# Kernel tuning notes

Measured on AMD Instinct MI355X. Metric: run time of the kernel, lower is better.

The kernel has to match this reference:

```python
import jax, jax.numpy as jnp
import numpy as np

THRESH = 0.5   # matching_threshold
EPS = 1e-8     # torch.cosine_similarity eps
LN_EPS = 1e-5

B, N = 32, 256
ID, PD, VD, SD = 2048, 768, 1024, 8


def _linear_block(x, w1, b1, w2, b2):
    # LinearBlock with linear_layer_num=2, dropout=0 (eval)
    h = jax.nn.relu(x @ w1 + b1)
    return h @ w2 + b2


def _layernorm(x, g, b):
    m = jnp.mean(x, axis=-1, keepdims=True)
    v = jnp.var(x, axis=-1, keepdims=True)
    return (x - m) / jnp.sqrt(v + LN_EPS) * g + b


def _greedy_match(sim_b, mask_b, prev_feat_b, prev_sp_b):
    # sim_b: [N, N] cosine similarities, mask_b: [N, N] bool
    n = sim_b.shape[0]
    iota = jnp.arange(n)

    def step(visited, inp):
        sim_i, mask_i = inp
        valid = mask_i & (~visited) & (sim_i >= THRESH)
        scores = jnp.where(valid, sim_i, -jnp.inf)
        idx = jnp.argmax(scores)          # first max, matching the torch loop
        found = jnp.any(valid)
        visited = visited | (found & (iota == idx))
        feat = jnp.where(found, prev_feat_b[idx], 0.0)
        sp = jnp.where(found, prev_sp_b[idx], 0.0)
        return visited, (feat, sp)

    _, (ofeat, osp) = jax.lax.scan(step, jnp.zeros((n,), bool), (sim_b, mask_b))
    return ofeat, osp


def setup_inputs() -> dict:
    key = jax.random.key(0)
    ks = jax.random.split(key, 32)
    s = 0.02
    inp = {
        'image_feature': jax.random.normal(ks[0], (B, N, ID), jnp.float32),
        'point_cloud_feature': jax.random.normal(ks[1], (B, N, PD), jnp.float32),
        'prev_image_feature': jax.random.normal(ks[2], (B, N, ID), jnp.float32),
        'prev_point_cloud_feature': jax.random.normal(ks[3], (B, N, PD), jnp.float32),
        'prev_spatial': jax.random.normal(ks[4], (B, N, SD), jnp.float32),
        'rel_dist_mask': jax.random.randint(ks[5], (B, N, N), 0, 2).astype(bool),
        # img_fusion: LinearBlock(2*ID, ID) -> Linear(ID, VD) -> LayerNorm(VD)
        'iw1': jax.random.normal(ks[6], (2 * ID, ID), jnp.float32) * s,
        'ib1': jnp.zeros((ID,), jnp.float32),
        'iw2': jax.random.normal(ks[7], (ID, ID), jnp.float32) * s,
        'ib2': jnp.zeros((ID,), jnp.float32),
        'iw3': jax.random.normal(ks[8], (ID, VD), jnp.float32) * s,
        'ib3': jnp.zeros((VD,), jnp.float32),
        'ig': jnp.ones((VD,), jnp.float32),
        'ibeta': jnp.zeros((VD,), jnp.float32),
        # pc_fusion: LinearBlock(2*PD, PD) -> Linear(PD, VD) -> LayerNorm(VD)
        'pw1': jax.random.normal(ks[9], (2 * PD, PD), jnp.float32) * s,
        'pb1': jnp.zeros((PD,), jnp.float32),
        'pw2': jax.random.normal(ks[10], (PD, PD), jnp.float32) * s,
        'pb2': jnp.zeros((PD,), jnp.float32),
        'pw3': jax.random.normal(ks[11], (PD, VD), jnp.float32) * s,
        'pb3': jnp.zeros((VD,), jnp.float32),
        'pg': jnp.ones((VD,), jnp.float32),
        'pbeta': jnp.zeros((VD,), jnp.float32),
        # linear: LinearBlock(2*VD, VD) -> LayerNorm(VD)
        'fw1': jax.random.normal(ks[12], (2 * VD, VD), jnp.float32) * s,
        'fb1': jnp.zeros((VD,), jnp.float32),
        'fw2': jax.random.normal(ks[13], (VD, VD), jnp.float32) * s,
        'fb2': jnp.zeros((VD,), jnp.float32),
        'fg': jnp.ones((VD,), jnp.float32),
        'fbeta': jnp.zeros((VD,), jnp.float32),
    }
    return inp


def reference(image_feature, point_cloud_feature, prev_image_feature,
              prev_point_cloud_feature, prev_spatial, rel_dist_mask,
              iw1, ib1, iw2, ib2, iw3, ib3, ig, ibeta,
              pw1, pb1, pw2, pb2, pw3, pb3, pg, pbeta,
              fw1, fb1, fw2, fb2, fg, fbeta):
    # ---- matching_previous_objects (batched cosine sim + greedy scan) ----
    feat = jnp.concatenate([image_feature, point_cloud_feature], axis=2)       # [B,N,D]
    prev_feat = jnp.concatenate([prev_image_feature, prev_point_cloud_feature], axis=2)
    fn = feat / jnp.maximum(jnp.linalg.norm(feat, axis=-1, keepdims=True), EPS)
    pn = prev_feat / jnp.maximum(jnp.linalg.norm(prev_feat, axis=-1, keepdims=True), EPS)
    sim = jnp.einsum('bid,bjd->bij', fn, pn)                                    # [B,N,N]
    ordered_prev, new_prev_spatial = jax.vmap(_greedy_match)(
        sim, rel_dist_mask, prev_feat, prev_spatial)
    prev_img = ordered_prev[:, :, :ID]
    prev_pc = ordered_prev[:, :, ID:]
    # ---- fusion MLPs ----
    img = jnp.concatenate([image_feature, prev_img], axis=2)
    img = _layernorm(_linear_block(img, iw1, ib1, iw2, ib2) @ iw3 + ib3, ig, ibeta)
    pc = jnp.concatenate([point_cloud_feature, prev_pc], axis=2)
    pc = _layernorm(_linear_block(pc, pw1, pb1, pw2, pb2) @ pw3 + pb3, pg, pbeta)
    vis = jnp.concatenate([img, pc], axis=2)
    vis = _layernorm(_linear_block(vis, fw1, fb1, fw2, fb2), fg, fbeta)
    return vis, new_prev_spatial
```

## Files before the change

### kernel.cpp

```cpp
#include <hip/hip_runtime.h>
#include <math.h>

#define Bn 32
#define Nn 256
#define IDIM 2048
#define PDIM 768
#define VDIM 1024
#define SDIM 8
#define D2 2816
#define Mrows 8192
#define EPSN 1e-8f
#define LNEPS 1e-5f
#define THRESH 0.5f

typedef unsigned short u16;
typedef __attribute__((ext_vector_type(8))) short bf16x8;
typedef __attribute__((ext_vector_type(4))) float f32x4;

__device__ __forceinline__ u16 f2b(float f) {
    unsigned u = __float_as_uint(f);
    unsigned r = (u + 0x7FFFu + ((u >> 16) & 1u)) >> 16;
    return (u16)r;
}

__device__ __forceinline__ void gload16(const void* g, void* l) {
    __builtin_amdgcn_global_load_lds(
        (const __attribute__((address_space(1))) unsigned*)g,
        (__attribute__((address_space(3))) unsigned*)l, 16, 0, 0);
}

#define VMWAIT4 asm volatile("s_waitcnt vmcnt(4)" ::: "memory")
#define VMWAIT2 asm volatile("s_waitcnt vmcnt(2)" ::: "memory")
#define VMWAIT0 asm volatile("s_waitcnt vmcnt(0)" ::: "memory")
#define BAR() do { __builtin_amdgcn_s_barrier(); __builtin_amdgcn_sched_barrier(0); } while (0)
#define PRIO1 __builtin_amdgcn_s_setprio(1)
#define PRIO0 __builtin_amdgcn_s_setprio(0)

__global__ __launch_bounds__(256) void pack_k(
    const float* __restrict__ img, const float* __restrict__ pc,
    const float* __restrict__ pimg, const float* __restrict__ ppc,
    u16* __restrict__ featb, u16* __restrict__ pfeatb,
    float* __restrict__ nf, float* __restrict__ np_)
{
    const int row = blockIdx.x, t = threadIdx.x;
    const float* I = blockIdx.y ? pimg : img;
    const float* P = blockIdx.y ? ppc : pc;
    u16* O = blockIdx.y ? pfeatb : featb;
    float s = 0.f;
    const float4* I4 = (const float4*)(I + (size_t)row * IDIM);
    float4 a = I4[t * 2], b = I4[t * 2 + 1];
    s += a.x * a.x + a.y * a.y + a.z * a.z + a.w * a.w;
    s += b.x * b.x + b.y * b.y + b.z * b.z + b.w * b.w;
    u16* op = O + (size_t)row * D2 + t * 8;
    *(ushort4*)op       = make_ushort4(f2b(a.x), f2b(a.y), f2b(a.z), f2b(a.w));
    *(ushort4*)(op + 4) = make_ushort4(f2b(b.x), f2b(b.y), f2b(b.z), f2b(b.w));
    if (t < 192) {
        float4 c = ((const float4*)(P + (size_t)row * PDIM))[t];
        s += c.x * c.x + c.y * c.y + c.z * c.z + c.w * c.w;
        *(ushort4*)(O + (size_t)row * D2 + IDIM + t * 4) =
            make_ushort4(f2b(c.x), f2b(c.y), f2b(c.z), f2b(c.w));
    }
    for (int o = 32; o; o >>= 1) s += __shfl_down(s, o, 64);
    __shared__ float l4[4];
    if ((t & 63) == 0) l4[t >> 6] = s;
    __syncthreads();
    if (t == 0) (blockIdx.y ? np_ : nf)[row] = sqrtf(l4[0] + l4[1] + l4[2] + l4[3]);
}

__global__ __launch_bounds__(256) void twt_k(
    const float* __restrict__ W, u16* __restrict__ Wt, int K, int No)
{
    __shared__ float tb[32][33];
    const int tx = threadIdx.x & 31;
    const int ty = threadIdx.x >> 5;
    const int n0 = blockIdx.x * 32, k0 = blockIdx.y * 32;
#pragma unroll
    for (int qq = 0; qq < 4; ++qq)
        tb[ty + 8 * qq][tx] = W[(size_t)(k0 + ty + 8 * qq) * No + n0 + tx];
    __syncthreads();
#pragma unroll
    for (int qq = 0; qq < 4; ++qq)
        Wt[(size_t)(n0 + ty + 8 * qq) * K + k0 + tx] = f2b(tb[tx][ty + 8 * qq]);
}

template <int MODE, int RELU, int OUT>
__global__ __launch_bounds__(256) void mm_k(
    const u16* __restrict__ A, const u16* __restrict__ Aprev,
    const int* __restrict__ midx, const float* __restrict__ zbuf,
    int lda, int coff, int K1,
    const u16* __restrict__ Bt, int K,
    const float* __restrict__ bias,
    const float* __restrict__ nf, const float* __restrict__ np_,
    void* __restrict__ Cout, int ldc)
{
    __shared__ __align__(16) u16 Asm[4096];
    __shared__ __align__(16) u16 Bsm[4096];
    const int tid = threadIdx.x;
    const int wave = tid >> 6, lane = tid & 63;
    const int row0 = blockIdx.y * 128;
    const int cC0 = blockIdx.x * 128;
    const int brow0 = (OUT == 2 ? (row0 >> 8) * Nn : 0) + cC0;

    const int la = lane >> 2, q = lane & 3;
    const u16* pA0[2]; const u16* pB0[2];
    char* dstA[2]; char* dstB[2];
#pragma unroll
    for (int i = 0; i < 2; ++i) {
        int c = wave * 2 + i;
        int r = c * 16 + la;
        int sp = q ^ ((r >> 1) & 3);
        int grow = row0 + r;
        pA0[i] = A + (size_t)grow * lda + sp * 8;
        pB0[i] = Bt + (size_t)(brow0 + r) * K + sp * 8;
        dstA[i] = (char*)Asm + c * 1024;
        dstB[i] = (char*)Bsm + c * 1024;
    }

    const int wr = wave >> 1, wc = wave & 1;
    int aoff[4], boff[4];
#pragma unroll
    for (int m = 0; m < 4; ++m) {
        int r = wr * 64 + m * 16 + (lane & 15);
        aoff[m] = r * 64 + (((lane >> 4) ^ ((r >> 1) & 3)) << 4);
    }
#pragma unroll
    for (int n = 0; n < 4; ++n) {
        int c = wc * 64 + n * 16 + (lane & 15);
        boff[n] = c * 64 + (((lane >> 4) ^ ((c >> 1) & 3)) << 4);
    }

    f32x4 acc[4][4] = {};

    for (int k0 = 0; k0 < K; k0 += 32) {
#pragma unroll
        for (int i = 0; i < 2; ++i) {
            gload16(pA0[i] + k0, dstA[i]);
            gload16(pB0[i] + k0, dstB[i]);
        }
        __syncthreads();
        bf16x8 av[4], bv[4];
#pragma unroll
        for (int m = 0; m < 4; ++m) av[m] = *(const bf16x8*)((const char*)Asm + aoff[m]);
#pragma unroll
        for (int n = 0; n < 4; ++n) bv[n] = *(const bf16x8*)((const char*)Bsm + boff[n]);
#pragma unroll
        for (int m = 0; m < 4; ++m)
#pragma unroll
            for (int n = 0; n < 4; ++n)
                acc[m][n] = __builtin_amdgcn_mfma_f32_16x16x32_bf16(av[m], bv[n], acc[m][n], 0, 0, 0);
        __syncthreads();
    }

    const int rb = row0 + wr * 64;
    const int cl = cC0 + wc * 64 + (lane & 15);
    float sj[4];
#pragma unroll
    for (int n = 0; n < 4; ++n) {
        int bcol = brow0 + wc * 64 + n * 16 + (lane & 15);
        sj[n] = 1.f / fmaxf(np_[bcol], EPSN);
    }
#pragma unroll
    for (int m = 0; m < 4; ++m) {
#pragma unroll
        for (int n = 0; n < 4; ++n) {
            f32x4 v = acc[m][n];
#pragma unroll
            for (int rg = 0; rg < 4; ++rg) {
                int rr = rb + m * 16 + ((lane >> 4) << 2) + rg;
                float si = 1.f / fmaxf(nf[rr], EPSN);
                ((float*)Cout)[(size_t)rr * ldc + cl + n * 16] = v[rg] * si * sj[n];
            }
        }
    }
}

template <int MODE, int RELU, int OUT>
__global__ __launch_bounds__(512, 2) void mm8_k(
    const u16* __restrict__ A, const u16* __restrict__ Aprev,
    const int* __restrict__ midx, const u16* __restrict__ zb,
    int lda, int coff, int K1,
    const u16* __restrict__ Bt, int K,
    const float* __restrict__ bias,
    void* __restrict__ Cout, int ldc, int nblk)
{
    __shared__ __align__(16) u16 smem[65536];
    char* ldsv = (char*)smem;

    const int tid = threadIdx.x;
    const int wave = tid >> 6, lane = tid & 63;
    const int l15 = lane & 15, l4 = lane >> 4;
    const int wr = wave >> 2, wc = wave & 3;

    const int nwg = nblk * 32;
    const int orig = blockIdx.x;
    const int xcd = orig & 7, lid = orig >> 3;
    const int qq = nwg >> 3, rr8 = nwg & 7;
    const int swz = (xcd < rr8 ? xcd * (qq + 1) : rr8 * (qq + 1) + (xcd - rr8) * qq) + lid;
    const int row0 = (swz & 31) * 256;
    const int col0 = (swz >> 5) * 256;

    const u16* pA[2][2]; const u16* pA2[2][2]; const u16* pB[2][2];
    int cA8[2][2]; bool okA[2][2];
#pragma unroll
    for (int h = 0; h < 2; ++h)
#pragma unroll
        for (int i = 0; i < 2; ++i) {
            int lrow = (i * 512 + tid) >> 3;
            int r = h * 128 + lrow;
            int c = (tid & 7) ^ (lrow & 7);
            cA8[h][i] = c * 8;
            int grow = row0 + r;
            if (MODE == 0) {
                pA[h][i] = A + (size_t)grow * lda + c * 8;
                pA2[h][i] = nullptr; okA[h][i] = true;
            } else {
                pA[h][i] = A + (size_t)grow * lda + coff + c * 8;
                int jj = midx[grow];
                okA[h][i] = (jj >= 0);
                pA2[h][i] = okA[h][i]
                    ? (Aprev + (size_t)((grow & ~(Nn - 1)) + jj) * lda + coff + c * 8 - K1)
                    : (zb + c * 8);
            }
            pB[h][i] = Bt + (size_t)(col0 + r) * K + c * 8;
        }

#define STAGEA(h, kt, pp) do {                                                   \
    _Pragma("unroll")                                                            \
    for (int i_ = 0; i_ < 2; ++i_) {                                             \
        const u16* s_;                                                           \
        if (MODE == 0) s_ = pA[h][i_] + (kt);                                    \
        else {                                                                   \
            int gc_ = (kt) + cA8[h][i_];                                         \
            s_ = (gc_ < K1) ? (pA[h][i_] + (kt))                                 \
                            : (okA[h][i_] ? pA2[h][i_] + (kt) : pA2[h][i_]);     \
        }                                                                        \
        gload16(s_, ldsv + ((pp) * 32768 + (h) * 16384 + i_ * 8192 + wave * 1024)); \
    }                                                                            \
} while (0)

#define STAGEB(h, kt, pp) do {                                                   \
    _Pragma("unroll")                                                            \
    for (int i_ = 0; i_ < 2; ++i_)                                               \
        gload16(pB[h][i_] + (kt),                                                \
                ldsv + (65536 + (pp) * 32768 + (h) * 16384 + i_ * 8192 + wave * 1024)); \
} while (0)

    int aoffs[8][2], boffs[4][2];
#pragma unroll
    for (int m = 0; m < 8; ++m) {
        int r = m * 32 + wr * 16 + l15;
#pragma unroll
        for (int ks = 0; ks < 2; ++ks)
            aoffs[m][ks] = r * 128 + (((ks * 4 + l4) ^ (lane & 7)) << 4);
    }
#pragma unroll
    for (int n = 0; n < 4; ++n) {
        int r = n * 64 + wc * 16 + l15;
#pragma unroll
        for (int ks = 0; ks < 2; ++ks)
            boffs[n][ks] = r * 128 + (((ks * 4 + l4) ^ (lane & 7)) << 4);
    }

    bf16x8 avc[4][2], bvc[2][2];
    f32x4 acc[8][4] = {};

#define READA(mh, base) do {                                                     \
    _Pragma("unroll")                                                            \
    for (int m_ = 0; m_ < 4; ++m_) {                                             \
        avc[m_][0] = *(const bf16x8*)((base) + aoffs[(mh) * 4 + m_][0]);         \
        avc[m_][1] = *(const bf16x8*)((base) + aoffs[(mh) * 4 + m_][1]);         \
    }                                                                            \
} while (0)

#define READB(nh, base) do {                                                     \
    _Pragma("unroll")                                                            \
    for (int n_ = 0; n_ < 2; ++n_) {                                             \
        bvc[n_][0] = *(const bf16x8*)((base) + boffs[(nh) * 2 + n_][0]);         \
        bvc[n_][1] = *(const bf16x8*)((base) + boffs[(nh) * 2 + n_][1]);         \
    }                                                                            \
} while (0)

#define MFMA16(mh, nh) do {                                                      \
    _Pragma("unroll")                                                            \
    for (int ks_ = 0; ks_ < 2; ++ks_)                                            \
    _Pragma("unroll")                                                            \
    for (int m_ = 0; m_ < 4; ++m_)                                               \
    _Pragma("unroll")                                                            \
    for (int n_ = 0; n_ < 2; ++n_)                                               \
        acc[(mh) * 4 + m_][(nh) * 2 + n_] = __builtin_amdgcn_mfma_f32_16x16x32_bf16( \
            avc[m_][ks_], bvc[n_][ks_], acc[(mh) * 4 + m_][(nh) * 2 + n_], 0, 0, 0); \
} while (0)

    const int nt = K >> 6;

    STAGEA(0, 0, 0); STAGEB(0, 0, 0); STAGEA(1, 0, 0); STAGEB(1, 0, 0);

    int t = 0;
    for (; t < nt - 1; ++t) {
        const int p = t & 1;
        const char* bA = ldsv + p * 32768;
        const char* bB = ldsv + 65536 + p * 32768;
        const int kn = (t + 1) << 6;
        VMWAIT4; BAR();
        STAGEA(0, kn, p ^ 1);
        READA(0, bA); READB(0, bB);
        PRIO1; MFMA16(0, 0); PRIO0;
        VMWAIT4; BAR();
        STAGEB(0, kn, p ^ 1);
        READA(1, bA);
        PRIO1; MFMA16(1, 0); PRIO0;
        VMWAIT4; BAR();
        STAGEA(1, kn, p ^ 1);
        READB(1, bB);
        PRIO1; MFMA16(1, 1); PRIO0;
        BAR();
        STAGEB(1, kn, p ^ 1);
        READA(0, bA);
        PRIO1; MFMA16(0, 1); PRIO0;
    }
    {
        const int p = t & 1;
        const char* bA = ldsv + p * 32768;
        const char* bB = ldsv + 65536 + p * 32768;
        VMWAIT4; BAR(); READA(0, bA); READB(0, bB); PRIO1; MFMA16(0, 0); PRIO0;
        VMWAIT2; BAR(); READA(1, bA);               PRIO1; MFMA16(1, 0); PRIO0;
        VMWAIT0; BAR(); READB(1, bB);               PRIO1; MFMA16(1, 1); PRIO0;
        BAR();          READA(0, bA);               PRIO1; MFMA16(0, 1); PRIO0;
    }

#pragma unroll
    for (int n = 0; n < 4; ++n) {
        const int col = col0 + n * 64 + wc * 16 + l15;
        const float bz = bias[col];
#pragma unroll
        for (int m = 0; m < 8; ++m) {
#pragma unroll
            for (int rg = 0; rg < 4; ++rg) {
                int row = row0 + m * 32 + wr * 16 + l4 * 4 + rg;
                float x = acc[m][n][rg] + bz;
                if (RELU) x = fmaxf(x, 0.f);
                if (OUT == 0) ((u16*)Cout)[(size_t)row * ldc + col] = f2b(x);
                else          ((float*)Cout)[(size_t)row * ldc + col] = x;
            }
        }
    }
#undef STAGEA
#undef STAGEB
#undef READA
#undef READB
#undef MFMA16
}

__global__ __launch_bounds__(256) void match_k(
    const float* __restrict__ sim, const int* __restrict__ mask,
    const float* __restrict__ psp, int* __restrict__ midx,
    float* __restrict__ osp, float* __restrict__ zb)
{
    const int b = blockIdx.x;
    const int j = threadIdx.x;
    const int lane = j & 63, wid = j >> 6;
    __shared__ int vis[256];
    __shared__ unsigned long long wb[4];
    __shared__ float wv[4];
    __shared__ int wi[4];
    __shared__ int fidx_s;
    if (b == 0) zb[j] = 0.f;
    vis[j] = 0;
    __syncthreads();
    size_t rowoff = ((size_t)b * Nn) * Nn + j;
    float s = sim[rowoff];
    int mk = mask[rowoff];
    for (int i = 0; i < Nn; ++i) {
        float scur = s; int mkcur = mk;
        bool valid = mkcur && (!vis[j]) && (scur >= THRESH);
        if (i + 1 < Nn) {
            s = sim[rowoff + (size_t)(i + 1) * Nn];
            mk = mask[rowoff + (size_t)(i + 1) * Nn];
        }
        unsigned long long bal = __ballot(valid);
        if (lane == 0) wb[wid] = bal;
        __syncthreads();
        bool found = (wb[0] | wb[1] | wb[2] | wb[3]) != 0ULL;
        if (found) {
            float v = valid ? scur : -INFINITY;
            int idx = j;
            for (int o = 32; o; o >>= 1) {
                float v2 = __shfl_down(v, o, 64);
                int i2 = __shfl_down(idx, o, 64);
                if (v2 > v || (v2 == v && i2 < idx)) { v = v2; idx = i2; }
            }
            if (lane == 0) { wv[wid] = v; wi[wid] = idx; }
            __syncthreads();
            if (j == 0) {
                float bv = wv[0]; int bi = wi[0];
                for (int w = 1; w < 4; ++w)
                    if (wv[w] > bv || (wv[w] == bv && wi[w] < bi)) { bv = wv[w]; bi = wi[w]; }
                fidx_s = bi;
                vis[bi] = 1;
                midx[b * Nn + i] = bi;
            }
            __syncthreads();
            int fi = fidx_s;
            if (j < SDIM)
                osp[((size_t)b * Nn + i) * SDIM + j] = psp[((size_t)b * Nn + fi) * SDIM + j];
        } else {
            if (j == 0) midx[b * Nn + i] = -1;
            if (j < SDIM) osp[((size_t)b * Nn + i) * SDIM + j] = 0.f;
        }
        __syncthreads();
    }
}

template <int OB>
__global__ __launch_bounds__(256) void ln_k(
    const float* __restrict__ X, const float* __restrict__ g,
    const float* __restrict__ be, void* __restrict__ out,
    int ostride, int ooff)
{
    const int row = blockIdx.x, t = threadIdx.x;
    float4 v = *(const float4*)(X + (size_t)row * VDIM + t * 4);
    float s = v.x + v.y + v.z + v.w;
    __shared__ float l4[4];
    for (int o = 32; o; o >>= 1) s += __shfl_down(s, o, 64);
    if ((t & 63) == 0) l4[t >> 6] = s;
    __syncthreads();
    float mean = (l4[0] + l4[1] + l4[2] + l4[3]) * (1.f / VDIM);
    __syncthreads();
    float dx = v.x - mean, dy = v.y - mean, dz = v.z - mean, dw = v.w - mean;
    float qv = dx * dx + dy * dy + dz * dz + dw * dw;
    for (int o = 32; o; o >>= 1) qv += __shfl_down(qv, o, 64);
    if ((t & 63) == 0) l4[t >> 6] = qv;
    __syncthreads();
    float var = (l4[0] + l4[1] + l4[2] + l4[3]) * (1.f / VDIM);
    float rstd = rsqrtf(var + LNEPS);
    float4 gv = *(const float4*)(g + t * 4);
    float4 bv = *(const float4*)(be + t * 4);
    float ox = dx * rstd * gv.x + bv.x;
    float oy = dy * rstd * gv.y + bv.y;
    float oz = dz * rstd * gv.z + bv.z;
    float ow = dw * rstd * gv.w + bv.w;
    if (OB) {
        *(ushort4*)((u16*)out + (size_t)row * ostride + ooff + t * 4) =
            make_ushort4(f2b(ox), f2b(oy), f2b(oz), f2b(ow));
    } else {
        *(float4*)((float*)out + (size_t)row * ostride + ooff + t * 4) =
            make_float4(ox, oy, oz, ow);
    }
}

extern "C" void kernel_launch(void* const* d_in, const int* in_sizes, int n_in,
                              void* d_out, int out_size, void* d_ws, size_t ws_size,
                              hipStream_t stream)
{
    const float* image  = (const float*)d_in[0];
    const float* pcf    = (const float*)d_in[1];
    const float* pimage = (const float*)d_in[2];
    const float* ppcf   = (const float*)d_in[3];
    const float* psp    = (const float*)d_in[4];
    const int*   mask   = (const int*)d_in[5];
    const float* iw1 = (const float*)d_in[6];  const float* ib1 = (const float*)d_in[7];
    const float* iw2 = (const float*)d_in[8];  const float* ib2 = (const float*)d_in[9];
    const float* iw3 = (const float*)d_in[10]; const float* ib3 = (const float*)d_in[11];
    const float* ig  = (const float*)d_in[12]; const float* ibeta = (const float*)d_in[13];
    const float* pw1 = (const float*)d_in[14]; const float* pb1 = (const float*)d_in[15];
    const float* pw2 = (const float*)d_in[16]; const float* pb2 = (const float*)d_in[17];
    const float* pw3 = (const float*)d_in[18]; const float* pb3 = (const float*)d_in[19];
    const float* pg  = (const float*)d_in[20]; const float* pbeta = (const float*)d_in[21];
    const float* fw1 = (const float*)d_in[22]; const float* fb1 = (const float*)d_in[23];
    const float* fw2 = (const float*)d_in[24]; const float* fb2 = (const float*)d_in[25];
    const float* fg  = (const float*)d_in[26]; const float* fbeta = (const float*)d_in[27];

    float* out_vis = (float*)d_out;
    float* out_sp  = (float*)d_out + (size_t)Mrows * VDIM;

    char* w = (char*)d_ws;
    float* nf   = (float*)w; w += 32768;
    float* np_  = (float*)w; w += 32768;
    int*   midx = (int*)w;   w += 32768;
    u16*   Wt   = (u16*)w;   w += 16777216;
    u16*   featb  = (u16*)w; w += 46137344;
    u16*   pfeatb = (u16*)w; w += 46137344;
    char*  Creg = w; w += 33554432;
    char*  Dreg = w; w += 33554432;
    char*  Ereg = w; w += 33554432;

    float* zbuf = nf;
    float* sim  = (float*)Ereg;
    u16*   ph1b = (u16*)Creg;
    u16*   ph2b = (u16*)(Creg + 12582912);
    float* preLNpc = (float*)Ereg;
    u16*   visb = (u16*)Dreg;
    u16*   h1b  = (u16*)Creg;
    u16*   h2b  = (u16*)featb;
    float* preLNimg = (float*)pfeatb;
    u16*   fh1b = (u16*)pfeatb;
    float* preLNf = (float*)featb;

    pack_k<<<dim3(Mrows, 2), 256, 0, stream>>>(image, pcf, pimage, ppcf,
                                               featb, pfeatb, nf, np_);
    mm_k<0, 0, 2><<<dim3(2, 64), 256, 0, stream>>>(
        featb, nullptr, nullptr, nullptr, D2, 0, 0,
        pfeatb, D2, nullptr, nf, np_, sim, Nn);
    match_k<<<dim3(Bn), 256, 0, stream>>>(sim, mask, psp, midx, out_sp, zbuf);

    twt_k<<<dim3(PDIM / 32, (2 * PDIM) / 32), 256, 0, stream>>>(pw1, Wt, 2 * PDIM, PDIM);
    mm8_k<1, 1, 0><<<dim3(3 * 32), 512, 0, stream>>>(
        featb, pfeatb, midx, (const u16*)zbuf, D2, IDIM, PDIM,
        Wt, 2 * PDIM, pb1, ph1b, PDIM, 3);
    twt_k<<<dim3(PDIM / 32, PDIM / 32), 256, 0, stream>>>(pw2, Wt, PDIM, PDIM);
    mm8_k<0, 0, 0><<<dim3(3 * 32), 512, 0, stream>>>(
        ph1b, nullptr, nullptr, nullptr, PDIM, 0, 0,
        Wt, PDIM, pb2, ph2b, PDIM, 3);
    twt_k<<<dim3(VDIM / 32, PDIM / 32), 256, 0, stream>>>(pw3, Wt, PDIM, VDIM);
    mm8_k<0, 0, 1><<<dim3(4 * 32), 512, 0, stream>>>(
        ph2b, nullptr, nullptr, nullptr, PDIM, 0, 0,
        Wt, PDIM, pb3, preLNpc, VDIM, 4);
    ln_k<1><<<dim3(Mrows), 256, 0, stream>>>(preLNpc, pg, pbeta, visb, 2048, 1024);

    twt_k<<<dim3(IDIM / 32, (2 * IDIM) / 32), 256, 0, stream>>>(iw1, Wt, 2 * IDIM, IDIM);
    mm8_k<1, 1, 0><<<dim3(8 * 32), 512, 0, stream>>>(
        featb, pfeatb, midx, (const u16*)zbuf, D2, 0, IDIM,
        Wt, 2 * IDIM, ib1, h1b, IDIM, 8);
    twt_k<<<dim3(IDIM / 32, IDIM / 32), 256, 0, stream>>>(iw2, Wt, IDIM, IDIM);
    mm8_k<0, 0, 0><<<dim3(8 * 32), 512, 0, stream>>>(
        h1b, nullptr, nullptr, nullptr, IDIM, 0, 0,
        Wt, IDIM, ib2, h2b, IDIM, 8);
    twt_k<<<dim3(VDIM / 32, IDIM / 32), 256, 0, stream>>>(iw3, Wt, IDIM, VDIM);
    mm8_k<0, 0, 1><<<dim3(4 * 32), 512, 0, stream>>>(
        h2b, nullptr, nullptr, nullptr, IDIM, 0, 0,
        Wt, IDIM, ib3, preLNimg, VDIM, 4);
    ln_k<1><<<dim3(Mrows), 256, 0, stream>>>(preLNimg, ig, ibeta, visb, 2048, 0);

    twt_k<<<dim3(VDIM / 32, 2048 / 32), 256, 0, stream>>>(fw1, Wt, 2048, VDIM);
    mm8_k<0, 1, 0><<<dim3(4 * 32), 512, 0, stream>>>(
        visb, nullptr, nullptr, nullptr, 2048, 0, 0,
        Wt, 2048, fb1, fh1b, VDIM, 4);
    twt_k<<<dim3(VDIM / 32, VDIM / 32), 256, 0, stream>>>(fw2, Wt, VDIM, VDIM);
    mm8_k<0, 0, 1><<<dim3(4 * 32), 512, 0, stream>>>(
        fh1b, nullptr, nullptr, nullptr, VDIM, 0, 0,
        Wt, VDIM, fb2, preLNf, VDIM, 4);
    ln_k<0><<<dim3(Mrows), 256, 0, stream>>>(preLNf, fg, fbeta, out_vis, VDIM, 0);
}
```

Baseline: 965.7 us.

## Group weight transposes and branch GEMMs; bitmask-based greedy matching

All eight weight transpose-to-bf16 launches are merged into one grouped kernel with per-segment descriptors. The image and point-cloud MLP GEMMs at each layer are now launched together as one grouped kernel, which fills more CUs than the smaller separate launches. The two branch LayerNorms are merged into one launch. The sequential greedy matcher is split into a parallel candidate-bitmask pass and a single-wave sequential pass that skips rows with no candidates and uses 64-bit visited masks instead of block-wide syncs. This needs a larger workspace to hold all transposed weights at once, and the grouped GEMMs pay for runtime descriptor selection.

```diff
diff --git a/kernel.cpp b/kernel.cpp
--- a/kernel.cpp
+++ b/kernel.cpp
@@ -14,6 +14,7 @@
 #define THRESH 0.5f
 
 typedef unsigned short u16;
+typedef unsigned long long u64;
 typedef __attribute__((ext_vector_type(8))) short bf16x8;
 typedef __attribute__((ext_vector_type(4))) float f32x4;
 
@@ -67,31 +68,41 @@
     if (t == 0) (blockIdx.y ? np_ : nf)[row] = sqrtf(l4[0] + l4[1] + l4[2] + l4[3]);
 }
 
-__global__ __launch_bounds__(256) void twt_k(
-    const float* __restrict__ W, u16* __restrict__ Wt, int K, int No)
-{
+struct TD { const float* W; u16* Wt; int K, No, blk0; };
+
+__global__ __launch_bounds__(256) void twtg_k(
+    TD a0, TD a1, TD a2, TD a3, TD a4, TD a5, TD a6, TD a7)
+{
+    const int bid = blockIdx.x;
+    TD d;
+    if      (bid >= a7.blk0) d = a7;
+    else if (bid >= a6.blk0) d = a6;
+    else if (bid >= a5.blk0) d = a5;
+    else if (bid >= a4.blk0) d = a4;
+    else if (bid >= a3.blk0) d = a3;
+    else if (bid >= a2.blk0) d = a2;
+    else if (bid >= a1.blk0) d = a1;
+    else                     d = a0;
+    const int local = bid - d.blk0;
+    const int nx = d.No >> 5;
+    const int n0 = (local % nx) * 32, k0 = (local / nx) * 32;
+
     __shared__ float tb[32][33];
     const int tx = threadIdx.x & 31;
     const int ty = threadIdx.x >> 5;
-    const int n0 = blockIdx.x * 32, k0 = blockIdx.y * 32;
 #pragma unroll
     for (int qq = 0; qq < 4; ++qq)
-        tb[ty + 8 * qq][tx] = W[(size_t)(k0 + ty + 8 * qq) * No + n0 + tx];
+        tb[ty + 8 * qq][tx] = d.W[(size_t)(k0 + ty + 8 * qq) * d.No + n0 + tx];
     __syncthreads();
 #pragma unroll
     for (int qq = 0; qq < 4; ++qq)
-        Wt[(size_t)(n0 + ty + 8 * qq) * K + k0 + tx] = f2b(tb[tx][ty + 8 * qq]);
-}
-
-template <int MODE, int RELU, int OUT>
-__global__ __launch_bounds__(256) void mm_k(
-    const u16* __restrict__ A, const u16* __restrict__ Aprev,
-    const int* __restrict__ midx, const float* __restrict__ zbuf,
-    int lda, int coff, int K1,
-    const u16* __restrict__ Bt, int K,
-    const float* __restrict__ bias,
+        d.Wt[(size_t)(n0 + ty + 8 * qq) * d.K + k0 + tx] = f2b(tb[tx][ty + 8 * qq]);
+}
+
+__global__ __launch_bounds__(256) void simmm_k(
+    const u16* __restrict__ A, const u16* __restrict__ Bt,
     const float* __restrict__ nf, const float* __restrict__ np_,
-    void* __restrict__ Cout, int ldc)
+    float* __restrict__ Cout)
 {
     __shared__ __align__(16) u16 Asm[4096];
     __shared__ __align__(16) u16 Bsm[4096];
@@ -99,7 +110,8 @@
     const int wave = tid >> 6, lane = tid & 63;
     const int row0 = blockIdx.y * 128;
     const int cC0 = blockIdx.x * 128;
-    const int brow0 = (OUT == 2 ? (row0 >> 8) * Nn : 0) + cC0;
+    const int brow0 = (row0 >> 8) * Nn + cC0;
+    const int lda = D2, K = D2, ldc = Nn;
 
     const int la = lane >> 2, q = lane & 3;
     const u16* pA0[2]; const u16* pB0[2];
@@ -109,8 +121,7 @@
         int c = wave * 2 + i;
         int r = c * 16 + la;
         int sp = q ^ ((r >> 1) & 3);
-        int grow = row0 + r;
-        pA0[i] = A + (size_t)grow * lda + sp * 8;
+        pA0[i] = A + (size_t)(row0 + r) * lda + sp * 8;
         pB0[i] = Bt + (size_t)(brow0 + r) * K + sp * 8;
         dstA[i] = (char*)Asm + c * 1024;
         dstB[i] = (char*)Bsm + c * 1024;
@@ -130,7 +141,6 @@
     }
 
     f32x4 acc[4][4] = {};
-
     for (int k0 = 0; k0 < K; k0 += 32) {
 #pragma unroll
         for (int i = 0; i < 2; ++i) {
@@ -155,12 +165,10 @@
     const int cl = cC0 + wc * 64 + (lane & 15);
     float sj[4];
 #pragma unroll
-    for (int n = 0; n < 4; ++n) {
-        int bcol = brow0 + wc * 64 + n * 16 + (lane & 15);
-        sj[n] = 1.f / fmaxf(np_[bcol], EPSN);
-    }
-#pragma unroll
-    for (int m = 0; m < 4; ++m) {
+    for (int n = 0; n < 4; ++n)
+        sj[n] = 1.f / fmaxf(np_[brow0 + wc * 64 + n * 16 + (lane & 15)], EPSN);
+#pragma unroll
+    for (int m = 0; m < 4; ++m)
 #pragma unroll
         for (int n = 0; n < 4; ++n) {
             f32x4 v = acc[m][n];
@@ -168,36 +176,40 @@
             for (int rg = 0; rg < 4; ++rg) {
                 int rr = rb + m * 16 + ((lane >> 4) << 2) + rg;
                 float si = 1.f / fmaxf(nf[rr], EPSN);
-                ((float*)Cout)[(size_t)rr * ldc + cl + n * 16] = v[rg] * si * sj[n];
+                Cout[(size_t)rr * ldc + cl + n * 16] = v[rg] * si * sj[n];
             }
         }
-    }
-}
+}
+
+struct MMDesc {
+    const u16* A; const u16* Aprev; const u16* zb; const int* midx;
+    const u16* Bt; const float* bias; void* C;
+    int lda, coff, K1, K, ldc, nwg;
+};
 
 template <int MODE, int RELU, int OUT>
-__global__ __launch_bounds__(512, 2) void mm8_k(
-    const u16* __restrict__ A, const u16* __restrict__ Aprev,
-    const int* __restrict__ midx, const u16* __restrict__ zb,
-    int lda, int coff, int K1,
-    const u16* __restrict__ Bt, int K,
-    const float* __restrict__ bias,
-    void* __restrict__ Cout, int ldc, int nblk)
+__global__ __launch_bounds__(512, 2) void mmg_k(MMDesc da, MMDesc db, int split)
 {
     __shared__ __align__(16) u16 smem[65536];
     char* ldsv = (char*)smem;
+
+    const int bid = blockIdx.x;
+    const MMDesc d = (bid < split) ? da : db;
+    const int local = (bid < split) ? bid : (bid - split);
 
     const int tid = threadIdx.x;
     const int wave = tid >> 6, lane = tid & 63;
     const int l15 = lane & 15, l4 = lane >> 4;
     const int wr = wave >> 2, wc = wave & 3;
 
-    const int nwg = nblk * 32;
-    const int orig = blockIdx.x;
-    const int xcd = orig & 7, lid = orig >> 3;
+    const int nwg = d.nwg;
+    const int xcd = local & 7, lid = local >> 3;
     const int qq = nwg >> 3, rr8 = nwg & 7;
     const int swz = (xcd < rr8 ? xcd * (qq + 1) : rr8 * (qq + 1) + (xcd - rr8) * qq) + lid;
     const int row0 = (swz & 31) * 256;
     const int col0 = (swz >> 5) * 256;
+
+    const int K1 = d.K1, lda = d.lda, coff = d.coff, K = d.K;
 
     const u16* pA[2][2]; const u16* pA2[2][2]; const u16* pB[2][2];
     int cA8[2][2]; bool okA[2][2];
@@ -211,17 +223,17 @@
             cA8[h][i] = c * 8;
             int grow = row0 + r;
             if (MODE == 0) {
-                pA[h][i] = A + (size_t)grow * lda + c * 8;
+                pA[h][i] = d.A + (size_t)grow * lda + c * 8;
                 pA2[h][i] = nullptr; okA[h][i] = true;
             } else {
-                pA[h][i] = A + (size_t)grow * lda + coff + c * 8;
-                int jj = midx[grow];
+                pA[h][i] = d.A + (size_t)grow * lda + coff + c * 8;
+                int jj = d.midx[grow];
                 okA[h][i] = (jj >= 0);
                 pA2[h][i] = okA[h][i]
-                    ? (Aprev + (size_t)((grow & ~(Nn - 1)) + jj) * lda + coff + c * 8 - K1)
-                    : (zb + c * 8);
+                    ? (d.Aprev + (size_t)((grow & ~(Nn - 1)) + jj) * lda + coff + c * 8 - K1)
+                    : (d.zb + c * 8);
             }
-            pB[h][i] = Bt + (size_t)(col0 + r) * K + c * 8;
+            pB[h][i] = d.Bt + (size_t)(col0 + r) * K + c * 8;
         }
 
 #define STAGEA(h, kt, pp) do {                                                   \
@@ -331,7 +343,7 @@
 #pragma unroll
     for (int n = 0; n < 4; ++n) {
         const int col = col0 + n * 64 + wc * 16 + l15;
-        const float bz = bias[col];
+        const float bz = d.bias[col];
 #pragma unroll
         for (int m = 0; m < 8; ++m) {
 #pragma unroll
@@ -339,8 +351,8 @@
                 int row = row0 + m * 32 + wr * 16 + l4 * 4 + rg;
                 float x = acc[m][n][rg] + bz;
                 if (RELU) x = fmaxf(x, 0.f);
-                if (OUT == 0) ((u16*)Cout)[(size_t)row * ldc + col] = f2b(x);
-                else          ((float*)Cout)[(size_t)row * ldc + col] = x;
+                if (OUT == 0) ((u16*)d.C)[(size_t)row * d.ldc + col] = f2b(x);
+                else          ((float*)d.C)[(size_t)row * d.ldc + col] = x;
             }
         }
     }
@@ -351,71 +363,94 @@
 #undef MFMA16
 }
 
-__global__ __launch_bounds__(256) void match_k(
+__global__ __launch_bounds__(256) void cand_k(
     const float* __restrict__ sim, const int* __restrict__ mask,
+    u64* __restrict__ cand, int* __restrict__ midx,
+    float* __restrict__ osp, float* __restrict__ zb)
+{
+    const int row = blockIdx.x, j = threadIdx.x;
+    size_t off = (size_t)row * Nn + j;
+    bool p = mask[off] && (sim[off] >= THRESH);
+    u64 bal = __ballot(p);
+    if ((j & 63) == 0) cand[row * 4 + (j >> 6)] = bal;
+    if (j == 0) midx[row] = -1;
+    if (j < SDIM) osp[(size_t)row * SDIM + j] = 0.f;
+    if (row == 0) zb[j] = 0.f;
+}
+
+__global__ __launch_bounds__(64) void matchseq_k(
+    const float* __restrict__ sim, const u64* __restrict__ cand,
     const float* __restrict__ psp, int* __restrict__ midx,
-    float* __restrict__ osp, float* __restrict__ zb)
+    float* __restrict__ osp)
 {
     const int b = blockIdx.x;
-    const int j = threadIdx.x;
-    const int lane = j & 63, wid = j >> 6;
-    __shared__ int vis[256];
-    __shared__ unsigned long long wb[4];
-    __shared__ float wv[4];
-    __shared__ int wi[4];
-    __shared__ int fidx_s;
-    if (b == 0) zb[j] = 0.f;
-    vis[j] = 0;
-    __syncthreads();
-    size_t rowoff = ((size_t)b * Nn) * Nn + j;
-    float s = sim[rowoff];
-    int mk = mask[rowoff];
+    const int lane = threadIdx.x;
+    __shared__ u64 cl[Nn * 4];
+    for (int k = lane; k < Nn * 4; k += 64) cl[k] = cand[b * Nn * 4 + k];
+    u64 vis = 0;
     for (int i = 0; i < Nn; ++i) {
-        float scur = s; int mkcur = mk;
-        bool valid = mkcur && (!vis[j]) && (scur >= THRESH);
-        if (i + 1 < Nn) {
-            s = sim[rowoff + (size_t)(i + 1) * Nn];
-            mk = mask[rowoff + (size_t)(i + 1) * Nn];
+        u64 c = (lane < 4) ? (cl[i * 4 + lane] & ~vis) : 0ull;
+        if (!__any(c != 0ull)) continue;
+        u64 cw = __shfl(c, lane >> 4, 64);
+        int basebit = (lane & 15) * 4;
+        float best = -INFINITY; int bidx = Nn;
+        const float* srow = sim + ((size_t)b * Nn + i) * Nn;
+#pragma unroll
+        for (int k = 0; k < 4; ++k) {
+            if ((cw >> (basebit + k)) & 1ull) {
+                int j = (lane >> 4) * 64 + basebit + k;
+                float v = srow[j];
+                if (v > best || (v == best && j < bidx)) { best = v; bidx = j; }
+            }
         }
-        unsigned long long bal = __ballot(valid);
-        if (lane == 0) wb[wid] = bal;
-        __syncthreads();
-        bool found = (wb[0] | wb[1] | wb[2] | wb[3]) != 0ULL;
-        if (found) {
-            float v = valid ? scur : -INFINITY;
-            int idx = j;
-            for (int o = 32; o; o >>= 1) {
-                float v2 = __shfl_down(v, o, 64);
-                int i2 = __shfl_down(idx, o, 64);
-                if (v2 > v || (v2 == v && i2 < idx)) { v = v2; idx = i2; }
-            }
-            if (lane == 0) { wv[wid] = v; wi[wid] = idx; }
-            __syncthreads();
-            if (j == 0) {
-                float bv = wv[0]; int bi = wi[0];
-                for (int w = 1; w < 4; ++w)
-                    if (wv[w] > bv || (wv[w] == bv && wi[w] < bi)) { bv = wv[w]; bi = wi[w]; }
-                fidx_s = bi;
-                vis[bi] = 1;
-                midx[b * Nn + i] = bi;
-            }
-            __syncthreads();
-            int fi = fidx_s;
-            if (j < SDIM)
-                osp[((size_t)b * Nn + i) * SDIM + j] = psp[((size_t)b * Nn + fi) * SDIM + j];
-        } else {
-            if (j == 0) midx[b * Nn + i] = -1;
-            if (j < SDIM) osp[((size_t)b * Nn + i) * SDIM + j] = 0.f;
+        for (int o = 32; o; o >>= 1) {
+            float v2 = __shfl_down(best, o, 64);
+            int i2 = __shfl_down(bidx, o, 64);
+            if (v2 > best || (v2 == best && i2 < bidx)) { best = v2; bidx = i2; }
         }
-        __syncthreads();
-    }
-}
-
-template <int OB>
-__global__ __launch_bounds__(256) void ln_k(
+        int jstar = __shfl(bidx, 0, 64);
+        if (lane == (jstar >> 6)) vis |= 1ull << (jstar & 63);
+        if (lane == 0) midx[b * Nn + i] = jstar;
+        if (lane < SDIM)
+            osp[((size_t)b * Nn + i) * SDIM + lane] = psp[((size_t)b * Nn + jstar) * SDIM + lane];
+    }
+}
+
+__global__ __launch_bounds__(256) void ln2_k(
+    const float* __restrict__ Xi, const float* __restrict__ gi, const float* __restrict__ bi,
+    const float* __restrict__ Xp, const float* __restrict__ gp, const float* __restrict__ bp,
+    u16* __restrict__ out)
+{
+    const int row = blockIdx.x, t = threadIdx.x;
+    const float* X = blockIdx.y ? Xp : Xi;
+    const float* g = blockIdx.y ? gp : gi;
+    const float* be = blockIdx.y ? bp : bi;
+    const int ooff = blockIdx.y ? VDIM : 0;
+    float4 v = *(const float4*)(X + (size_t)row * VDIM + t * 4);
+    float s = v.x + v.y + v.z + v.w;
+    __shared__ float l4[4];
+    for (int o = 32; o; o >>= 1) s += __shfl_down(s, o, 64);
+    if ((t & 63) == 0) l4[t >> 6] = s;
+    __syncthreads();
+    float mean = (l4[0] + l4[1] + l4[2] + l4[3]) * (1.f / VDIM);
+    __syncthreads();
+    float dx = v.x - mean, dy = v.y - mean, dz = v.z - mean, dw = v.w - mean;
+    float qv = dx * dx + dy * dy + dz * dz + dw * dw;
+    for (int o = 32; o; o >>= 1) qv += __shfl_down(qv, o, 64);
+    if ((t & 63) == 0) l4[t >> 6] = qv;
+    __syncthreads();
+    float var = (l4[0] + l4[1] + l4[2] + l4[3]) * (1.f / VDIM);
+    float rstd = rsqrtf(var + LNEPS);
+    float4 gv = *(const float4*)(g + t * 4);
+    float4 bv = *(const float4*)(be + t * 4);
+    *(ushort4*)(out + (size_t)row * 2048 + ooff + t * 4) = make_ushort4(
+        f2b(dx * rstd * gv.x + bv.x), f2b(dy * rstd * gv.y + bv.y),
+        f2b(dz * rstd * gv.z + bv.z), f2b(dw * rstd * gv.w + bv.w));
+}
+
+__global__ __launch_bounds__(256) void lnf_k(
     const float* __restrict__ X, const float* __restrict__ g,
-    const float* __restrict__ be, void* __restrict__ out,
-    int ostride, int ooff)
+    const float* __restrict__ be, float* __restrict__ out)
 {
     const int row = blockIdx.x, t = threadIdx.x;
     float4 v = *(const float4*)(X + (size_t)row * VDIM + t * 4);
@@ -435,17 +470,9 @@
     float rstd = rsqrtf(var + LNEPS);
     float4 gv = *(const float4*)(g + t * 4);
     float4 bv = *(const float4*)(be + t * 4);
-    float ox = dx * rstd * gv.x + bv.x;
-    float oy = dy * rstd * gv.y + bv.y;
-    float oz = dz * rstd * gv.z + bv.z;
-    float ow = dw * rstd * gv.w + bv.w;
-    if (OB) {
-        *(ushort4*)((u16*)out + (size_t)row * ostride + ooff + t * 4) =
-            make_ushort4(f2b(ox), f2b(oy), f2b(oz), f2b(ow));
-    } else {
-        *(float4*)((float*)out + (size_t)row * ostride + ooff + t * 4) =
-            make_float4(ox, oy, oz, ow);
-    }
+    *(float4*)(out + (size_t)row * VDIM + t * 4) = make_float4(
+        dx * rstd * gv.x + bv.x, dy * rstd * gv.y + bv.y,
+        dz * rstd * gv.z + bv.z, dw * rstd * gv.w + bv.w);
 }
 
 extern "C" void kernel_launch(void* const* d_in, const int* in_sizes, int n_in,
@@ -473,71 +500,88 @@
     float* out_vis = (float*)d_out;
     float* out_sp  = (float*)d_out + (size_t)Mrows * VDIM;
 
-    char* w = (char*)d_ws;
-    float* nf   = (float*)w; w += 32768;
-    float* np_  = (float*)w; w += 32768;
-    int*   midx = (int*)w;   w += 32768;
-    u16*   Wt   = (u16*)w;   w += 16777216;
-    u16*   featb  = (u16*)w; w += 46137344;
-    u16*   pfeatb = (u16*)w; w += 46137344;
-    char*  Creg = w; w += 33554432;
-    char*  Dreg = w; w += 33554432;
-    char*  Ereg = w; w += 33554432;
-
-    float* zbuf = nf;
-    float* sim  = (float*)Ereg;
-    u16*   ph1b = (u16*)Creg;
-    u16*   ph2b = (u16*)(Creg + 12582912);
-    float* preLNpc = (float*)Ereg;
-    u16*   visb = (u16*)Dreg;
-    u16*   h1b  = (u16*)Creg;
-    u16*   h2b  = (u16*)featb;
-    float* preLNimg = (float*)pfeatb;
-    u16*   fh1b = (u16*)pfeatb;
-    float* preLNf = (float*)featb;
+    char* wsb = (char*)d_ws;
+    float* nf   = (float*)(wsb + 0);
+    float* np_  = (float*)(wsb + 32768);
+    int*   midx = (int*)(wsb + 65536);
+    u64*   cand = (u64*)(wsb + 98304);
+    u16*   wt0  = (u16*)(wsb + 524288);
+    u16* iw1t = wt0;
+    u16* iw2t = wt0 + 8388608;
+    u16* iw3t = wt0 + 12582912;
+    u16* pw1t = wt0 + 14680064;
+    u16* pw2t = wt0 + 15859712;
+    u16* pw3t = wt0 + 16449536;
+    u16* fw1t = wt0 + 17235968;
+    u16* fw2t = wt0 + 19333120;
+    char* R1 = wsb + 41287680;
+    char* R2 = wsb + 87425024;
+    char* R3 = wsb + 133562368;
+    char* R4 = wsb + 167116800;
+
+    u16*   featb   = (u16*)R1;
+    u16*   pfeatb  = (u16*)R2;
+    float* sim     = (float*)R3;
+    u16*   h1b     = (u16*)R3;
+    u16*   ph1b    = (u16*)R4;
+    u16*   h2b     = (u16*)R1;
+    u16*   ph2b    = (u16*)(R1 + 33554432);
+    float* preLNimg = (float*)R2;
+    float* preLNpc  = (float*)R4;
+    u16*   visb    = (u16*)R3;
+    u16*   fh1b    = (u16*)R4;
+    float* preLNf  = (float*)R3;
+    float* zbuf    = nf;
 
     pack_k<<<dim3(Mrows, 2), 256, 0, stream>>>(image, pcf, pimage, ppcf,
                                                featb, pfeatb, nf, np_);
-    mm_k<0, 0, 2><<<dim3(2, 64), 256, 0, stream>>>(
-        featb, nullptr, nullptr, nullptr, D2, 0, 0,
-        pfeatb, D2, nullptr, nf, np_, sim, Nn);
-    match_k<<<dim3(Bn), 256, 0, stream>>>(sim, mask, psp, midx, out_sp, zbuf);
-
-    twt_k<<<dim3(PDIM / 32, (2 * PDIM) / 32), 256, 0, stream>>>(pw1, Wt, 2 * PDIM, PDIM);
-    mm8_k<1, 1, 0><<<dim3(3 * 32), 512, 0, stream>>>(
-        featb, pfeatb, midx, (const u16*)zbuf, D2, IDIM, PDIM,
-        Wt, 2 * PDIM, pb1, ph1b, PDIM, 3);
-    twt_k<<<dim3(PDIM / 32, PDIM / 32), 256, 0, stream>>>(pw2, Wt, PDIM, PDIM);
-    mm8_k<0, 0, 0><<<dim3(3 * 32), 512, 0, stream>>>(
-        ph1b, nullptr, nullptr, nullptr, PDIM, 0, 0,
-        Wt, PDIM, pb2, ph2b, PDIM, 3);
-    twt_k<<<dim3(VDIM / 32, PDIM / 32), 256, 0, stream>>>(pw3, Wt, PDIM, VDIM);
-    mm8_k<0, 0, 1><<<dim3(4 * 32), 512, 0, stream>>>(
-        ph2b, nullptr, nullptr, nullptr, PDIM, 0, 0,
-        Wt, PDIM, pb3, preLNpc, VDIM, 4);
-    ln_k<1><<<dim3(Mrows), 256, 0, stream>>>(preLNpc, pg, pbeta, visb, 2048, 1024);
-
-    twt_k<<<dim3(IDIM / 32, (2 * IDIM) / 32), 256, 0, stream>>>(iw1, Wt, 2 * IDIM, IDIM);
-    mm8_k<1, 1, 0><<<dim3(8 * 32), 512, 0, stream>>>(
-        featb, pfeatb, midx, (const u16*)zbuf, D2, 0, IDIM,
-        Wt, 2 * IDIM, ib1, h1b, IDIM, 8);
-    twt_k<<<dim3(IDIM / 32, IDIM / 32), 256, 0, stream>>>(iw2, Wt, IDIM, IDIM);
-    mm8_k<0, 0, 0><<<dim3(8 * 32), 512, 0, stream>>>(
-        h1b, nullptr, nullptr, nullptr, IDIM, 0, 0,
-        Wt, IDIM, ib2, h2b, IDIM, 8);
-    twt_k<<<dim3(VDIM / 32, IDIM / 32), 256, 0, stream>>>(iw3, Wt, IDIM, VDIM);
-    mm8_k<0, 0, 1><<<dim3(4 * 32), 512, 0, stream>>>(
-        h2b, nullptr, nullptr, nullptr, IDIM, 0, 0,
-        Wt, IDIM, ib3, preLNimg, VDIM, 4);
-    ln_k<1><<<dim3(Mrows), 256, 0, stream>>>(preLNimg, ig, ibeta, visb, 2048, 0);
-
-    twt_k<<<dim3(VDIM / 32, 2048 / 32), 256, 0, stream>>>(fw1, Wt, 2048, VDIM);
-    mm8_k<0, 1, 0><<<dim3(4 * 32), 512, 0, stream>>>(
-        visb, nullptr, nullptr, nullptr, 2048, 0, 0,
-        Wt, 2048, fb1, fh1b, VDIM, 4);
-    twt_k<<<dim3(VDIM / 32, VDIM / 32), 256, 0, stream>>>(fw2, Wt, VDIM, VDIM);
-    mm8_k<0, 0, 1><<<dim3(4 * 32), 512, 0, stream>>>(
-        fh1b, nullptr, nullptr, nullptr, VDIM, 0, 0,
-        Wt, VDIM, fb2, preLNf, VDIM, 4);
-    ln_k<0><<<dim3(Mrows), 256, 0, stream>>>(preLNf, fg, fbeta, out_vis, VDIM, 0);
-}
+    {
+        TD t0 = { iw1, iw1t, 2 * IDIM, IDIM, 0 };
+        TD t1 = { iw2, iw2t, IDIM, IDIM, 8192 };
+        TD t2 = { iw3, iw3t, IDIM, VDIM, 12288 };
+        TD t3 = { pw1, pw1t, 2 * PDIM, PDIM, 14336 };
+        TD t4 = { pw2, pw2t, PDIM, PDIM, 15488 };
+        TD t5 = { pw3, pw3t, PDIM, VDIM, 16064 };
+        TD t6 = { fw1, fw1t, 2048, VDIM, 16832 };
+        TD t7 = { fw2, fw2t, VDIM, VDIM, 18880 };
+        twtg_k<<<dim3(19904), 256, 0, stream>>>(t0, t1, t2, t3, t4, t5, t6, t7);
+    }
+    simmm_k<<<dim3(2, 64), 256, 0, stream>>>(featb, pfeatb, nf, np_, sim);
+    cand_k<<<dim3(Mrows), 256, 0, stream>>>(sim, mask, cand, midx, out_sp, zbuf);
+    matchseq_k<<<dim3(Bn), 64, 0, stream>>>(sim, cand, psp, midx, out_sp);
+
+    {
+        MMDesc di = { featb, pfeatb, (const u16*)zbuf, midx, iw1t, ib1, h1b,
+                      D2, 0, IDIM, 2 * IDIM, IDIM, 256 };
+        MMDesc dp = { featb, pfeatb, (const u16*)zbuf, midx, pw1t, pb1, ph1b,
+                      D2, IDIM, PDIM, 2 * PDIM, PDIM, 96 };
+        mmg_k<1, 1, 0><<<dim3(352), 512, 0, stream>>>(di, dp, 256);
+    }
+    {
+        MMDesc di = { h1b, nullptr, nullptr, nullptr, iw2t, ib2, h2b,
+                      IDIM, 0, 0, IDIM, IDIM, 256 };
+        MMDesc dp = { ph1b, nullptr, nullptr, nullptr, pw2t, pb2, ph2b,
+                      PDIM, 0, 0, PDIM, PDIM, 96 };
+        mmg_k<0, 0, 0><<<dim3(352), 512, 0, stream>>>(di, dp, 256);
+    }
+    {
+        MMDesc di = { h2b, nullptr, nullptr, nullptr, iw3t, ib3, preLNimg,
+                      IDIM, 0, 0, IDIM, VDIM, 128 };
+        MMDesc dp = { ph2b, nullptr, nullptr, nullptr, pw3t, pb3, preLNpc,
+                      PDIM, 0, 0, PDIM, VDIM, 128 };
+        mmg_k<0, 0, 1><<<dim3(256), 512, 0, stream>>>(di, dp, 128);
+    }
+    ln2_k<<<dim3(Mrows, 2), 256, 0, stream>>>(preLNimg, ig, ibeta,
+                                              preLNpc, pg, pbeta, visb);
+    {
+        MMDesc df = { visb, nullptr, nullptr, nullptr, fw1t, fb1, fh1b,
+                      2048, 0, 0, 2048, VDIM, 128 };
+        mmg_k<0, 1, 0><<<dim3(128), 512, 0, stream>>>(df, df, 128);
+    }
+    {
+        MMDesc df = { fh1b, nullptr, nullptr, nullptr, fw2t, fb2, preLNf,
+                      VDIM, 0, 0, VDIM, VDIM, 128 };
+        mmg_k<0, 0, 1><<<dim3(128), 512, 0, stream>>>(df, df, 128);
+    }
+    lnf_k<<<dim3(Mrows), 256, 0, stream>>>(preLNf, fg, fbeta, out_vis);
+}
```

Result: faster. 819.2 us (-15.2%).
